# Kernel tuning notes

Hardware: AMD Instinct MI355X
Metric: run time of the kernel (lower is better)

Reference implementation:

```python
import jax, jax.numpy as jnp
import numpy as np

B, T, D = 4, 2048, 512
H, DK = 8, 64  # n_head, d_kv; inner_dim = H*DK = 512


def setup_inputs() -> dict:
    key = jax.random.key(0)
    ks = jax.random.split(key, 6)
    s = 1.0 / np.sqrt(D)
    return {
        "x": jax.random.normal(ks[0], (B, T, D), dtype=jnp.float32),
        "mask": jnp.zeros((B, 1, 1, T), dtype=jnp.float32),
        "position_bias": jax.random.normal(ks[1], (1, H, T, T), dtype=jnp.float32),
        "Wq": jax.random.normal(ks[2], (D, D), dtype=jnp.float32) * s,
        "Wk": jax.random.normal(ks[3], (D, D), dtype=jnp.float32) * s,
        "Wv": jax.random.normal(ks[4], (D, D), dtype=jnp.float32) * s,
        "Wo": jax.random.normal(ks[5], (D, D), dtype=jnp.float32) * s,
    }


def reference(x, mask, position_bias, Wq, Wk, Wv, Wo):
    # Linear projections (torch nn.Linear: y = x @ W.T), split into heads.
    q = (x @ Wq.T).reshape(B, T, H, DK).transpose(0, 2, 1, 3)  # [B,H,T,DK]
    k = (x @ Wk.T).reshape(B, T, H, DK).transpose(0, 2, 1, 3)  # [B,H,S,DK]
    v = (x @ Wv.T).reshape(B, T, H, DK).transpose(0, 2, 1, 3)  # [B,H,S,DK]
    # T5: no 1/sqrt(d_k) scaling; additive position bias + mask before softmax.
    scores = jnp.einsum("bhtd,bhsd->bhts", q, k) + position_bias + mask
    attn = jax.nn.softmax(scores.astype(jnp.float32), axis=-1).astype(q.dtype)
    # dropout is identity at inference
    y = jnp.einsum("bhts,bhsd->bhtd", attn, v)  # [B,H,T,DK]
    y = y.transpose(0, 2, 1, 3).reshape(B, T, H * DK)
    return y @ Wo.T
```

## Files before the change

kernel.cpp:

```cpp
#include <hip/hip_runtime.h>
#include <stdint.h>

typedef unsigned short u16;
typedef __attribute__((ext_vector_type(8))) _Float16 half8;
typedef __attribute__((ext_vector_type(4))) float f32x4;

#define L2E 1.4426950408889634f

#define NTOK 8192
#define DIM  512
#define TT   2048

__device__ __forceinline__ u16 f2h(float f) {
  _Float16 h = (_Float16)f;
  return __builtin_bit_cast(u16, h);
}

__device__ __forceinline__ void async16(const void* g, void* l) {
  __builtin_amdgcn_global_load_lds(
      (const __attribute__((address_space(1))) unsigned int*)g,
      (__attribute__((address_space(3))) unsigned int*)l, 16, 0, 0);
}

__global__ __launch_bounds__(256) void k_convert(
    const float* __restrict__ x, const float* __restrict__ wq,
    const float* __restrict__ wk, const float* __restrict__ wv,
    const float* __restrict__ wo, u16* __restrict__ xb) {
  size_t i = ((size_t)blockIdx.x * 256 + threadIdx.x) * 8;
  const float* src;
  u16* dst;
  size_t off;
  if (i < 4194304) {
    src = x; dst = xb; off = i;
  } else {
    size_t j = i - 4194304;
    int w = (int)(j >> 18);
    off = j & 262143;
    src = (w == 0) ? wq : (w == 1) ? wk : (w == 2) ? wv : wo;
    dst = xb + 4194304 + (size_t)w * 262144;
  }
  float4 a = *(const float4*)(src + off);
  float4 b = *(const float4*)(src + off + 4);
  uint4 pk;
  pk.x = (unsigned)f2h(a.x) | ((unsigned)f2h(a.y) << 16);
  pk.y = (unsigned)f2h(a.z) | ((unsigned)f2h(a.w) << 16);
  pk.z = (unsigned)f2h(b.x) | ((unsigned)f2h(b.y) << 16);
  pk.w = (unsigned)f2h(b.z) | ((unsigned)f2h(b.w) << 16);
  *(uint4*)(dst + off) = pk;
}

template <int MODE>
__global__ __launch_bounds__(256) void k_gemm(
    const u16* __restrict__ A, const u16* __restrict__ Wb,
    u16* __restrict__ Db, float* __restrict__ Df) {
  const int tid = threadIdx.x;
  const int wave = tid >> 6, lane = tid & 63;
  const int quad = lane >> 4, l16 = lane & 15;
  const int wr = wave >> 1, wc = wave & 1;
  const int m0 = blockIdx.x * 128, n0 = blockIdx.y * 128;

  const u16* W = Wb;
  u16* D = Db;
  int vmode = 0;
  if (MODE == 0) {
    int z = blockIdx.z;
    W = Wb + (size_t)z * 262144;
    D = Db + (size_t)z * 4194304;
    vmode = (z == 2);
  }

  __shared__ __align__(16) u16 As[128 * 64];
  __shared__ __align__(16) u16 Bs[128 * 64];

  f32x4 acc[4][4];
  for (int rt = 0; rt < 4; ++rt)
    for (int ct = 0; ct < 4; ++ct) acc[rt][ct] = (f32x4){0.f, 0.f, 0.f, 0.f};

  for (int kb = 0; kb < 8; ++kb) {
    const int k0 = kb * 64;
    for (int r = 0; r < 4; ++r) {
      int cid = r * 256 + tid;
      int row = cid >> 3, cl = cid & 7, cg = cl ^ (row & 7);
      async16(A + (size_t)(m0 + row) * DIM + k0 + cg * 8,
              &As[(r * 256 + wave * 64) * 8]);
    }
    for (int r = 0; r < 4; ++r) {
      int cid = r * 256 + tid;
      int row = cid >> 3, cl = cid & 7, cg = cl ^ (row & 7);
      async16(W + (size_t)(n0 + row) * DIM + k0 + cg * 8,
              &Bs[(r * 256 + wave * 64) * 8]);
    }
    __syncthreads();
    for (int kc = 0; kc < 2; ++kc) {
      half8 af[4], bfv[4];
      for (int rt = 0; rt < 4; ++rt) {
        int row = wr * 64 + rt * 16 + l16;
        int c = (kc * 4 + quad) ^ (row & 7);
        af[rt] = *(const half8*)&As[row * 64 + c * 8];
      }
      for (int ct = 0; ct < 4; ++ct) {
        int row = wc * 64 + ct * 16 + l16;
        int c = (kc * 4 + quad) ^ (row & 7);
        bfv[ct] = *(const half8*)&Bs[row * 64 + c * 8];
      }
      for (int rt = 0; rt < 4; ++rt)
        for (int ct = 0; ct < 4; ++ct)
          acc[rt][ct] = __builtin_amdgcn_mfma_f32_16x16x32_f16(
              af[rt], bfv[ct], acc[rt][ct], 0, 0, 0);
    }
    __syncthreads();
  }

  for (int rt = 0; rt < 4; ++rt)
    for (int ct = 0; ct < 4; ++ct)
      for (int reg = 0; reg < 4; ++reg) {
        int gm = m0 + wr * 64 + rt * 16 + quad * 4 + reg;
        int gn = n0 + wc * 64 + ct * 16 + l16;
        float v = acc[rt][ct][reg];
        if (MODE == 1) {
          Df[(size_t)gm * DIM + gn] = v;
        } else {
          int bb = gm >> 11, t = gm & 2047, hh = gn >> 6, dk = gn & 63;
          if (!vmode)
            D[(((size_t)(bb * 8 + hh) * TT + t) << 6) + dk] = f2h(v);
          else
            D[(((size_t)(bb * 8 + hh) << 6) + dk) * TT + t] = f2h(v);
        }
      }
}

__global__ __launch_bounds__(256) void k_attn(
    const u16* __restrict__ Q, const u16* __restrict__ K,
    const u16* __restrict__ Vt, const float* __restrict__ bias,
    const float* __restrict__ mask, u16* __restrict__ Y) {
  const int tid = threadIdx.x;
  const int wv = tid >> 6;
  const int lane = tid & 63;
  const int quad = lane >> 4;
  const int l16 = lane & 15;

  const int bx = blockIdx.x;
  const int bh = bx >> 4;
  const int qt = bx & 15;
  const int b = bh >> 3, h = bh & 7;
  const int q0 = qt * 128;

  __shared__ __align__(16) u16 Ks[64 * 64];
  __shared__ __align__(16) u16 Vs[64 * 64];
  __shared__ __align__(16) u16 Pl[128 * 72];

  half8 qf[2][2];
  for (int rt = 0; rt < 2; ++rt) {
    size_t qrow = (size_t)bh * TT + q0 + wv * 32 + rt * 16 + l16;
    for (int kc = 0; kc < 2; ++kc)
      qf[rt][kc] = *(const half8*)(Q + qrow * 64 + kc * 32 + quad * 8);
  }

  float m_i[2][4], l_i[2][4];
  f32x4 oacc[2][4];
  for (int rt = 0; rt < 2; ++rt)
    for (int r = 0; r < 4; ++r) { m_i[rt][r] = -1e30f; l_i[rt][r] = 0.f; }
  for (int rt = 0; rt < 2; ++rt)
    for (int ct = 0; ct < 4; ++ct) oacc[rt][ct] = (f32x4){0.f, 0.f, 0.f, 0.f};

  const size_t biasbase = (size_t)h * TT * TT;

  for (int st = 0; st < 32; ++st) {
    const int s0 = st * 64;
    for (int r = 0; r < 2; ++r) {
      int cid = r * 256 + tid;
      int row = cid >> 3, cl = cid & 7, cg = cl ^ (row & 7);
      async16(K + ((size_t)bh * TT + s0 + row) * 64 + cg * 8,
              &Ks[(r * 256 + wv * 64) * 8]);
      async16(Vt + ((size_t)(bh * 64 + row)) * TT + s0 + cg * 8,
              &Vs[(r * 256 + wv * 64) * 8]);
    }
    __syncthreads();

    float mk[4];
    for (int ct = 0; ct < 4; ++ct) mk[ct] = mask[b * TT + s0 + ct * 16 + l16];

    f32x4 sacc[2][4];
    for (int rt = 0; rt < 2; ++rt)
      for (int ct = 0; ct < 4; ++ct) sacc[rt][ct] = (f32x4){0.f, 0.f, 0.f, 0.f};
    for (int kc = 0; kc < 2; ++kc) {
      half8 bfv[4];
      for (int ct = 0; ct < 4; ++ct) {
        int row = ct * 16 + l16;
        int c = (kc * 4 + quad) ^ (row & 7);
        bfv[ct] = *(const half8*)&Ks[row * 64 + c * 8];
      }
      for (int rt = 0; rt < 2; ++rt)
        for (int ct = 0; ct < 4; ++ct)
          sacc[rt][ct] = __builtin_amdgcn_mfma_f32_16x16x32_f16(
              qf[rt][kc], bfv[ct], sacc[rt][ct], 0, 0, 0);
    }

    float bv[2][4][4];
    for (int rt = 0; rt < 2; ++rt) {
      int tg = q0 + wv * 32 + rt * 16 + quad * 4;
      for (int reg = 0; reg < 4; ++reg) {
        const float* bp = bias + biasbase + (size_t)(tg + reg) * TT + s0 + l16;
        for (int ct = 0; ct < 4; ++ct) bv[rt][ct][reg] = bp[ct * 16];
      }
    }

    for (int rt = 0; rt < 2; ++rt) {
      for (int reg = 0; reg < 4; ++reg) {
        float s[4];
        for (int ct = 0; ct < 4; ++ct)
          s[ct] = sacc[rt][ct][reg] + bv[rt][ct][reg] + mk[ct];
        float mx = fmaxf(fmaxf(s[0], s[1]), fmaxf(s[2], s[3]));
        mx = fmaxf(mx, __shfl_xor(mx, 1));
        mx = fmaxf(mx, __shfl_xor(mx, 2));
        mx = fmaxf(mx, __shfl_xor(mx, 4));
        mx = fmaxf(mx, __shfl_xor(mx, 8));
        float mold = m_i[rt][reg];
        float mnew = fmaxf(mold, mx);
        float alpha = __builtin_amdgcn_exp2f((mold - mnew) * L2E);
        float p[4], rs = 0.f;
        for (int ct = 0; ct < 4; ++ct) {
          p[ct] = __builtin_amdgcn_exp2f((s[ct] - mnew) * L2E);
          rs += p[ct];
        }
        rs += __shfl_xor(rs, 1);
        rs += __shfl_xor(rs, 2);
        rs += __shfl_xor(rs, 4);
        rs += __shfl_xor(rs, 8);
        l_i[rt][reg] = l_i[rt][reg] * alpha + rs;
        m_i[rt][reg] = mnew;
        for (int ct = 0; ct < 4; ++ct) oacc[rt][ct][reg] *= alpha;
        int prow = wv * 32 + rt * 16 + quad * 4 + reg;
        for (int ct = 0; ct < 4; ++ct) Pl[prow * 72 + ct * 16 + l16] = f2h(p[ct]);
      }
    }
    __syncthreads();

    for (int kc = 0; kc < 2; ++kc) {
      half8 pf[2], vf[4];
      for (int rt = 0; rt < 2; ++rt)
        pf[rt] = *(const half8*)&Pl[(wv * 32 + rt * 16 + l16) * 72 + kc * 32 + quad * 8];
      for (int ct = 0; ct < 4; ++ct) {
        int row = ct * 16 + l16;
        int c = (kc * 4 + quad) ^ (row & 7);
        vf[ct] = *(const half8*)&Vs[row * 64 + c * 8];
      }
      for (int rt = 0; rt < 2; ++rt)
        for (int ct = 0; ct < 4; ++ct)
          oacc[rt][ct] = __builtin_amdgcn_mfma_f32_16x16x32_f16(
              pf[rt], vf[ct], oacc[rt][ct], 0, 0, 0);
    }
    __syncthreads();
  }

  for (int rt = 0; rt < 2; ++rt)
    for (int reg = 0; reg < 4; ++reg) {
      int tg = q0 + wv * 32 + rt * 16 + quad * 4 + reg;
      float inv = 1.f / l_i[rt][reg];
      for (int ct = 0; ct < 4; ++ct) {
        float v = oacc[rt][ct][reg] * inv;
        Y[((size_t)(b * TT + tg)) * DIM + h * 64 + ct * 16 + l16] = f2h(v);
      }
    }
}

extern "C" void kernel_launch(void* const* d_in, const int* in_sizes, int n_in,
                              void* d_out, int out_size, void* d_ws, size_t ws_size,
                              hipStream_t stream) {
  const float* x    = (const float*)d_in[0];
  const float* mask = (const float*)d_in[1];
  const float* bias = (const float*)d_in[2];
  const float* Wq   = (const float*)d_in[3];
  const float* Wk   = (const float*)d_in[4];
  const float* Wv   = (const float*)d_in[5];
  const float* Wo   = (const float*)d_in[6];
  (void)Wk; (void)Wv;

  u16* xb  = (u16*)d_ws;
  u16* wb  = xb + 4194304;
  u16* qkv = wb + 4 * 262144;
  u16* yb  = qkv + 3 * (size_t)4194304;

  k_convert<<<2560, 256, 0, stream>>>(x, Wq, Wk, Wv, Wo, xb);
  k_gemm<0><<<dim3(64, 4, 3), 256, 0, stream>>>(xb, wb, qkv, nullptr);
  k_attn<<<512, 256, 0, stream>>>(qkv, qkv + 4194304, qkv + 2 * (size_t)4194304,
                                  bias, mask, yb);
  k_gemm<1><<<dim3(64, 4, 1), 256, 0, stream>>>(yb, wb + 3 * 262144, nullptr,
                                                (float*)d_out);
}
```

Before: 343.6 us.

## Halve attention and output GEMM tiles, swap MFMA operands for V-transpose store

The attention kernel now uses 64-query tiles (one 16-row tile per wave) and launches twice as many blocks. The output projection gets its own kernel with 64-row tiles and twice the grid, and the V projection moves to a separate launch. That launch swaps the MFMA operands so the transposed V store writes consecutive tokens per lane and coalesces. The smaller tiles are meant to raise occupancy and block count, at the cost of loading K/V tiles twice as often per query and adding one kernel launch.

```diff
diff --git a/kernel.cpp b/kernel.cpp
--- a/kernel.cpp
+++ b/kernel.cpp
@@ -49,24 +49,25 @@
   *(uint4*)(dst + off) = pk;
 }
 
-template <int MODE>
-__global__ __launch_bounds__(256) void k_gemm(
+template <bool VSWAP>
+__global__ __launch_bounds__(256) void k_proj(
     const u16* __restrict__ A, const u16* __restrict__ Wb,
-    u16* __restrict__ Db, float* __restrict__ Df) {
+    u16* __restrict__ Db) {
   const int tid = threadIdx.x;
   const int wave = tid >> 6, lane = tid & 63;
   const int quad = lane >> 4, l16 = lane & 15;
   const int wr = wave >> 1, wc = wave & 1;
   const int m0 = blockIdx.x * 128, n0 = blockIdx.y * 128;
 
-  const u16* W = Wb;
-  u16* D = Db;
-  int vmode = 0;
-  if (MODE == 0) {
+  const u16* W;
+  u16* D;
+  if (VSWAP) {
+    W = Wb + 2 * 262144;
+    D = Db + 2 * (size_t)4194304;
+  } else {
     int z = blockIdx.z;
     W = Wb + (size_t)z * 262144;
     D = Db + (size_t)z * 4194304;
-    vmode = (z == 2);
   }
 
   __shared__ __align__(16) u16 As[128 * 64];
@@ -92,7 +93,7 @@
     }
     __syncthreads();
     for (int kc = 0; kc < 2; ++kc) {
-      half8 af[4], bfv[4];
+      half8 af[4], wf[4];
       for (int rt = 0; rt < 4; ++rt) {
         int row = wr * 64 + rt * 16 + l16;
         int c = (kc * 4 + quad) ^ (row & 7);
@@ -101,12 +102,15 @@
       for (int ct = 0; ct < 4; ++ct) {
         int row = wc * 64 + ct * 16 + l16;
         int c = (kc * 4 + quad) ^ (row & 7);
-        bfv[ct] = *(const half8*)&Bs[row * 64 + c * 8];
+        wf[ct] = *(const half8*)&Bs[row * 64 + c * 8];
       }
       for (int rt = 0; rt < 4; ++rt)
         for (int ct = 0; ct < 4; ++ct)
-          acc[rt][ct] = __builtin_amdgcn_mfma_f32_16x16x32_f16(
-              af[rt], bfv[ct], acc[rt][ct], 0, 0, 0);
+          acc[rt][ct] = VSWAP
+              ? __builtin_amdgcn_mfma_f32_16x16x32_f16(wf[ct], af[rt],
+                                                       acc[rt][ct], 0, 0, 0)
+              : __builtin_amdgcn_mfma_f32_16x16x32_f16(af[rt], wf[ct],
+                                                       acc[rt][ct], 0, 0, 0);
     }
     __syncthreads();
   }
@@ -114,18 +118,78 @@
   for (int rt = 0; rt < 4; ++rt)
     for (int ct = 0; ct < 4; ++ct)
       for (int reg = 0; reg < 4; ++reg) {
-        int gm = m0 + wr * 64 + rt * 16 + quad * 4 + reg;
+        float v = acc[rt][ct][reg];
+        if (!VSWAP) {
+          int gm = m0 + wr * 64 + rt * 16 + quad * 4 + reg;
+          int gn = n0 + wc * 64 + ct * 16 + l16;
+          int bb = gm >> 11, t = gm & 2047, hh = gn >> 6, dk = gn & 63;
+          D[(((size_t)(bb * 8 + hh) * TT + t) << 6) + dk] = f2h(v);
+        } else {
+          int feat = n0 + wc * 64 + ct * 16 + quad * 4 + reg;
+          int tok  = m0 + wr * 64 + rt * 16 + l16;
+          int bb = tok >> 11, t = tok & 2047, hh = feat >> 6, dk = feat & 63;
+          D[(((size_t)(bb * 8 + hh) << 6) + dk) * TT + t] = f2h(v);
+        }
+      }
+}
+
+__global__ __launch_bounds__(256) void k_ogemm(
+    const u16* __restrict__ A, const u16* __restrict__ W,
+    float* __restrict__ Df) {
+  const int tid = threadIdx.x;
+  const int wave = tid >> 6, lane = tid & 63;
+  const int quad = lane >> 4, l16 = lane & 15;
+  const int wr = wave >> 1, wc = wave & 1;
+  const int m0 = blockIdx.x * 64, n0 = blockIdx.y * 128;
+
+  __shared__ __align__(16) u16 As[64 * 64];
+  __shared__ __align__(16) u16 Bs[128 * 64];
+
+  f32x4 acc[2][4];
+  for (int rt = 0; rt < 2; ++rt)
+    for (int ct = 0; ct < 4; ++ct) acc[rt][ct] = (f32x4){0.f, 0.f, 0.f, 0.f};
+
+  for (int kb = 0; kb < 8; ++kb) {
+    const int k0 = kb * 64;
+    for (int r = 0; r < 2; ++r) {
+      int cid = r * 256 + tid;
+      int row = cid >> 3, cl = cid & 7, cg = cl ^ (row & 7);
+      async16(A + (size_t)(m0 + row) * DIM + k0 + cg * 8,
+              &As[(r * 256 + wave * 64) * 8]);
+    }
+    for (int r = 0; r < 4; ++r) {
+      int cid = r * 256 + tid;
+      int row = cid >> 3, cl = cid & 7, cg = cl ^ (row & 7);
+      async16(W + (size_t)(n0 + row) * DIM + k0 + cg * 8,
+              &Bs[(r * 256 + wave * 64) * 8]);
+    }
+    __syncthreads();
+    for (int kc = 0; kc < 2; ++kc) {
+      half8 af[2], wf[4];
+      for (int rt = 0; rt < 2; ++rt) {
+        int row = wr * 32 + rt * 16 + l16;
+        int c = (kc * 4 + quad) ^ (row & 7);
+        af[rt] = *(const half8*)&As[row * 64 + c * 8];
+      }
+      for (int ct = 0; ct < 4; ++ct) {
+        int row = wc * 64 + ct * 16 + l16;
+        int c = (kc * 4 + quad) ^ (row & 7);
+        wf[ct] = *(const half8*)&Bs[row * 64 + c * 8];
+      }
+      for (int rt = 0; rt < 2; ++rt)
+        for (int ct = 0; ct < 4; ++ct)
+          acc[rt][ct] = __builtin_amdgcn_mfma_f32_16x16x32_f16(
+              af[rt], wf[ct], acc[rt][ct], 0, 0, 0);
+    }
+    __syncthreads();
+  }
+
+  for (int rt = 0; rt < 2; ++rt)
+    for (int ct = 0; ct < 4; ++ct)
+      for (int reg = 0; reg < 4; ++reg) {
+        int gm = m0 + wr * 32 + rt * 16 + quad * 4 + reg;
         int gn = n0 + wc * 64 + ct * 16 + l16;
-        float v = acc[rt][ct][reg];
-        if (MODE == 1) {
-          Df[(size_t)gm * DIM + gn] = v;
-        } else {
-          int bb = gm >> 11, t = gm & 2047, hh = gn >> 6, dk = gn & 63;
-          if (!vmode)
-            D[(((size_t)(bb * 8 + hh) * TT + t) << 6) + dk] = f2h(v);
-          else
-            D[(((size_t)(bb * 8 + hh) << 6) + dk) * TT + t] = f2h(v);
-        }
+        Df[(size_t)gm * DIM + gn] = acc[rt][ct][reg];
       }
 }
 
@@ -140,28 +204,26 @@
   const int l16 = lane & 15;
 
   const int bx = blockIdx.x;
-  const int bh = bx >> 4;
-  const int qt = bx & 15;
+  const int bh = bx >> 5;
+  const int qt = bx & 31;
   const int b = bh >> 3, h = bh & 7;
-  const int q0 = qt * 128;
+  const int q0 = qt * 64;
 
   __shared__ __align__(16) u16 Ks[64 * 64];
   __shared__ __align__(16) u16 Vs[64 * 64];
-  __shared__ __align__(16) u16 Pl[128 * 72];
-
-  half8 qf[2][2];
-  for (int rt = 0; rt < 2; ++rt) {
-    size_t qrow = (size_t)bh * TT + q0 + wv * 32 + rt * 16 + l16;
+  __shared__ __align__(16) u16 Pl[64 * 72];
+
+  half8 qf[2];
+  {
+    size_t qrow = (size_t)bh * TT + q0 + wv * 16 + l16;
     for (int kc = 0; kc < 2; ++kc)
-      qf[rt][kc] = *(const half8*)(Q + qrow * 64 + kc * 32 + quad * 8);
-  }
-
-  float m_i[2][4], l_i[2][4];
-  f32x4 oacc[2][4];
-  for (int rt = 0; rt < 2; ++rt)
-    for (int r = 0; r < 4; ++r) { m_i[rt][r] = -1e30f; l_i[rt][r] = 0.f; }
-  for (int rt = 0; rt < 2; ++rt)
-    for (int ct = 0; ct < 4; ++ct) oacc[rt][ct] = (f32x4){0.f, 0.f, 0.f, 0.f};
+      qf[kc] = *(const half8*)(Q + qrow * 64 + kc * 32 + quad * 8);
+  }
+
+  float m_i[4], l_i[4];
+  f32x4 oacc[4];
+  for (int r = 0; r < 4; ++r) { m_i[r] = -1e30f; l_i[r] = 0.f; }
+  for (int ct = 0; ct < 4; ++ct) oacc[ct] = (f32x4){0.f, 0.f, 0.f, 0.f};
 
   const size_t biasbase = (size_t)h * TT * TT;
 
@@ -180,88 +242,81 @@
     float mk[4];
     for (int ct = 0; ct < 4; ++ct) mk[ct] = mask[b * TT + s0 + ct * 16 + l16];
 
-    f32x4 sacc[2][4];
-    for (int rt = 0; rt < 2; ++rt)
-      for (int ct = 0; ct < 4; ++ct) sacc[rt][ct] = (f32x4){0.f, 0.f, 0.f, 0.f};
+    f32x4 sacc[4];
+    for (int ct = 0; ct < 4; ++ct) sacc[ct] = (f32x4){0.f, 0.f, 0.f, 0.f};
     for (int kc = 0; kc < 2; ++kc) {
-      half8 bfv[4];
+      half8 kf[4];
       for (int ct = 0; ct < 4; ++ct) {
         int row = ct * 16 + l16;
         int c = (kc * 4 + quad) ^ (row & 7);
-        bfv[ct] = *(const half8*)&Ks[row * 64 + c * 8];
-      }
-      for (int rt = 0; rt < 2; ++rt)
-        for (int ct = 0; ct < 4; ++ct)
-          sacc[rt][ct] = __builtin_amdgcn_mfma_f32_16x16x32_f16(
-              qf[rt][kc], bfv[ct], sacc[rt][ct], 0, 0, 0);
-    }
-
-    float bv[2][4][4];
-    for (int rt = 0; rt < 2; ++rt) {
-      int tg = q0 + wv * 32 + rt * 16 + quad * 4;
+        kf[ct] = *(const half8*)&Ks[row * 64 + c * 8];
+      }
+      for (int ct = 0; ct < 4; ++ct)
+        sacc[ct] = __builtin_amdgcn_mfma_f32_16x16x32_f16(
+            qf[kc], kf[ct], sacc[ct], 0, 0, 0);
+    }
+
+    float bv[4][4];
+    {
+      int tg = q0 + wv * 16 + quad * 4;
       for (int reg = 0; reg < 4; ++reg) {
         const float* bp = bias + biasbase + (size_t)(tg + reg) * TT + s0 + l16;
-        for (int ct = 0; ct < 4; ++ct) bv[rt][ct][reg] = bp[ct * 16];
-      }
-    }
-
-    for (int rt = 0; rt < 2; ++rt) {
-      for (int reg = 0; reg < 4; ++reg) {
-        float s[4];
-        for (int ct = 0; ct < 4; ++ct)
-          s[ct] = sacc[rt][ct][reg] + bv[rt][ct][reg] + mk[ct];
-        float mx = fmaxf(fmaxf(s[0], s[1]), fmaxf(s[2], s[3]));
-        mx = fmaxf(mx, __shfl_xor(mx, 1));
-        mx = fmaxf(mx, __shfl_xor(mx, 2));
-        mx = fmaxf(mx, __shfl_xor(mx, 4));
-        mx = fmaxf(mx, __shfl_xor(mx, 8));
-        float mold = m_i[rt][reg];
-        float mnew = fmaxf(mold, mx);
-        float alpha = __builtin_amdgcn_exp2f((mold - mnew) * L2E);
-        float p[4], rs = 0.f;
-        for (int ct = 0; ct < 4; ++ct) {
-          p[ct] = __builtin_amdgcn_exp2f((s[ct] - mnew) * L2E);
-          rs += p[ct];
-        }
-        rs += __shfl_xor(rs, 1);
-        rs += __shfl_xor(rs, 2);
-        rs += __shfl_xor(rs, 4);
-        rs += __shfl_xor(rs, 8);
-        l_i[rt][reg] = l_i[rt][reg] * alpha + rs;
-        m_i[rt][reg] = mnew;
-        for (int ct = 0; ct < 4; ++ct) oacc[rt][ct][reg] *= alpha;
-        int prow = wv * 32 + rt * 16 + quad * 4 + reg;
-        for (int ct = 0; ct < 4; ++ct) Pl[prow * 72 + ct * 16 + l16] = f2h(p[ct]);
-      }
+        for (int ct = 0; ct < 4; ++ct) bv[ct][reg] = bp[ct * 16];
+      }
+    }
+
+    for (int reg = 0; reg < 4; ++reg) {
+      float s[4];
+      for (int ct = 0; ct < 4; ++ct)
+        s[ct] = sacc[ct][reg] + bv[ct][reg] + mk[ct];
+      float mx = fmaxf(fmaxf(s[0], s[1]), fmaxf(s[2], s[3]));
+      mx = fmaxf(mx, __shfl_xor(mx, 1));
+      mx = fmaxf(mx, __shfl_xor(mx, 2));
+      mx = fmaxf(mx, __shfl_xor(mx, 4));
+      mx = fmaxf(mx, __shfl_xor(mx, 8));
+      float mold = m_i[reg];
+      float mnew = fmaxf(mold, mx);
+      float alpha = __builtin_amdgcn_exp2f((mold - mnew) * L2E);
+      float p[4], rs = 0.f;
+      for (int ct = 0; ct < 4; ++ct) {
+        p[ct] = __builtin_amdgcn_exp2f((s[ct] - mnew) * L2E);
+        rs += p[ct];
+      }
+      rs += __shfl_xor(rs, 1);
+      rs += __shfl_xor(rs, 2);
+      rs += __shfl_xor(rs, 4);
+      rs += __shfl_xor(rs, 8);
+      l_i[reg] = l_i[reg] * alpha + rs;
+      m_i[reg] = mnew;
+      for (int ct = 0; ct < 4; ++ct) oacc[ct][reg] *= alpha;
+      int prow = wv * 16 + quad * 4 + reg;
+      for (int ct = 0; ct < 4; ++ct) Pl[prow * 72 + ct * 16 + l16] = f2h(p[ct]);
     }
     __syncthreads();
 
     for (int kc = 0; kc < 2; ++kc) {
-      half8 pf[2], vf[4];
-      for (int rt = 0; rt < 2; ++rt)
-        pf[rt] = *(const half8*)&Pl[(wv * 32 + rt * 16 + l16) * 72 + kc * 32 + quad * 8];
+      half8 pf, vf[4];
+      pf = *(const half8*)&Pl[(wv * 16 + l16) * 72 + kc * 32 + quad * 8];
       for (int ct = 0; ct < 4; ++ct) {
         int row = ct * 16 + l16;
         int c = (kc * 4 + quad) ^ (row & 7);
         vf[ct] = *(const half8*)&Vs[row * 64 + c * 8];
       }
-      for (int rt = 0; rt < 2; ++rt)
-        for (int ct = 0; ct < 4; ++ct)
-          oacc[rt][ct] = __builtin_amdgcn_mfma_f32_16x16x32_f16(
-              pf[rt], vf[ct], oacc[rt][ct], 0, 0, 0);
-    }
-    __syncthreads();
-  }
-
-  for (int rt = 0; rt < 2; ++rt)
-    for (int reg = 0; reg < 4; ++reg) {
-      int tg = q0 + wv * 32 + rt * 16 + quad * 4 + reg;
-      float inv = 1.f / l_i[rt][reg];
-      for (int ct = 0; ct < 4; ++ct) {
-        float v = oacc[rt][ct][reg] * inv;
-        Y[((size_t)(b * TT + tg)) * DIM + h * 64 + ct * 16 + l16] = f2h(v);
-      }
-    }
+      for (int ct = 0; ct < 4; ++ct)
+        oacc[ct] = __builtin_amdgcn_mfma_f32_16x16x32_f16(
+            pf, vf[ct], oacc[ct], 0, 0, 0);
+    }
+    __syncthreads();
+  }
+
+  for (int reg = 0; reg < 4; ++reg) {
+    int tg = q0 + wv * 16 + quad * 4 + reg;
+    float inv = 1.f / l_i[reg];
+    for (int ct = 0; ct < 4; ++ct) {
+      float v = oacc[ct][reg] * inv;
+      Y[((size_t)(b * TT + tg)) * DIM + h * 64 + ct * 16 + l16] = f2h(v);
+    }
+  }
 }
 
 extern "C" void kernel_launch(void* const* d_in, const int* in_sizes, int n_in,
@@ -282,9 +337,9 @@
   u16* yb  = qkv + 3 * (size_t)4194304;
 
   k_convert<<<2560, 256, 0, stream>>>(x, Wq, Wk, Wv, Wo, xb);
-  k_gemm<0><<<dim3(64, 4, 3), 256, 0, stream>>>(xb, wb, qkv, nullptr);
-  k_attn<<<512, 256, 0, stream>>>(qkv, qkv + 4194304, qkv + 2 * (size_t)4194304,
-                                  bias, mask, yb);
-  k_gemm<1><<<dim3(64, 4, 1), 256, 0, stream>>>(yb, wb + 3 * 262144, nullptr,
-                                                (float*)d_out);
-}
+  k_proj<false><<<dim3(64, 4, 2), 256, 0, stream>>>(xb, wb, qkv);
+  k_proj<true><<<dim3(64, 4), 256, 0, stream>>>(xb, wb, qkv);
+  k_attn<<<1024, 256, 0, stream>>>(qkv, qkv + 4194304,
+                                   qkv + 2 * (size_t)4194304, bias, mask, yb);
+  k_ogemm<<<dim3(128, 4), 256, 0, stream>>>(yb, wb + 3 * 262144, (float*)d_out);
+}
```

New measurement: 329.4 us. 1.04x faster.
